# Performance work log

Hardware: AMD Instinct MI355X
Metric: run time of the kernel (lower is better)

## Reference

```python
import math
import jax, jax.numpy as jnp
import numpy as np

B, S, D = 2, 2048, 1024
H = 8
HD = D // H // 2            # 64, per-branch head dim
ROT = HD // 2               # 32, rotary rot_dim (RotaryEmbedding dim=head_dim//2)
DEPTH = 2
LAMBDA_INIT = 0.8 - 0.6 * math.exp(-0.3 * DEPTH)


def rope(t):
    # t: (b, s, heads, HD); rotate first ROT dims with interleaved pairs
    s = t.shape[1]
    inv = 1.0 / (10000.0 ** (jnp.arange(0, ROT, 2, dtype=jnp.float32) / ROT))  # (ROT/2,)
    freqs = jnp.arange(s, dtype=jnp.float32)[:, None] * inv                    # (s, ROT/2)
    freqs = jnp.repeat(freqs, 2, axis=-1)                                      # (s, ROT)
    cos = jnp.cos(freqs)[None, :, None, :]
    sin = jnp.sin(freqs)[None, :, None, :]
    tl, tr = t[..., :ROT], t[..., ROT:]
    xp = tl.reshape(tl.shape[:-1] + (ROT // 2, 2))
    rh = jnp.stack((-xp[..., 1], xp[..., 0]), axis=-1).reshape(tl.shape)
    return jnp.concatenate([tl * cos + rh * sin, tr], axis=-1)


def rmsnorm(x, w, b, eps=1e-8):
    return x * jax.lax.rsqrt(jnp.mean(x * x, axis=-1, keepdims=True) + eps) * w + b


def layernorm(x, w, b, eps=1e-5):
    m = jnp.mean(x, axis=-1, keepdims=True)
    v = jnp.mean((x - m) ** 2, axis=-1, keepdims=True)
    return (x - m) * jax.lax.rsqrt(v + eps) * w + b


def causal_attn(q, k, v):
    # q,k: (b,s,h,dqk)  v: (b,s,h,dv) -> (b,s,h,dv); flash default scale 1/sqrt(dqk)
    s = q.shape[1]
    scores = jnp.einsum('bqhd,bkhd->bhqk', q, k) / jnp.sqrt(jnp.asarray(q.shape[-1], q.dtype))
    mask = jnp.tril(jnp.ones((s, s), dtype=bool))
    scores = jnp.where(mask, scores, jnp.asarray(-jnp.inf, scores.dtype))
    p = jax.nn.softmax(scores, axis=-1)
    return jnp.einsum('bhqk,bkhe->bqhe', p, v)


def setup_inputs() -> dict:
    key = jax.random.key(0)
    ks = jax.random.split(key, 16)
    f32 = jnp.float32
    inp = {
        'x': jax.random.normal(ks[0], (B, S, D), dtype=f32),
        'sigmas': jax.random.normal(ks[1], (B, HD), dtype=f32),
        'w_qkv': jax.random.normal(ks[2], (D, 3 * D), dtype=f32) * 0.02,
        'w_out': jax.random.normal(ks[3], (D, D), dtype=f32) * 0.02,
        'lq1': jax.random.normal(ks[4], (HD,), dtype=f32) * 0.1,
        'lk1': jax.random.normal(ks[5], (HD,), dtype=f32) * 0.1,
        'lq2': jax.random.normal(ks[6], (HD,), dtype=f32) * 0.1,
        'lk2': jax.random.normal(ks[7], (HD,), dtype=f32) * 0.1,
        'ln_w': jnp.ones((2 * HD,), f32) + 0.02 * jax.random.normal(ks[8], (2 * HD,), dtype=f32),
        'ln_b': 0.02 * jax.random.normal(ks[9], (2 * HD,), dtype=f32),
        'lnq_w': jnp.ones((HD,), f32) + 0.02 * jax.random.normal(ks[10], (HD,), dtype=f32),
        'lnq_b': 0.02 * jax.random.normal(ks[11], (HD,), dtype=f32),
        'ln1_w': jnp.ones((D,), f32), 'ln1_b': jnp.zeros((D,), f32),
        'ln2_w': jnp.ones((D,), f32), 'ln2_b': jnp.zeros((D,), f32),
        'w1': jax.random.normal(ks[12], (D, 4 * D), dtype=f32) * 0.02,
        'b1': jnp.zeros((4 * D,), f32),
        'w2': jax.random.normal(ks[13], (4 * D, D), dtype=f32) * 0.02,
        'b2': jnp.zeros((D,), f32),
    }
    return inp


def reference(x, sigmas, w_qkv, w_out, lq1, lk1, lq2, lk2, ln_w, ln_b,
              lnq_w, lnq_b, ln1_w, ln1_b, ln2_w, ln2_b, w1, b1, w2, b2):
    b, s, d = x.shape
    qkv = x @ w_qkv
    q, k, v = jnp.split(qkv, 3, axis=-1)
    q = q.reshape(b, s, 2 * H, HD)
    k = k.reshape(b, s, 2 * H, HD)
    v = v.reshape(b, s, H, 2 * HD)
    q = rope(q)
    k = rope(k)
    q = q.reshape(b, s, H, 2, HD)
    k = k.reshape(b, s, H, 2, HD)
    q1, q2 = q[..., 0, :], q[..., 1, :]
    k1, k2 = k[..., 0, :], k[..., 1, :]
    sig = sigmas[:, None, None, :]  # (b,1,1,HD)
    attn1 = causal_attn(q1, k1, v)
    attn2 = causal_attn(rmsnorm(q2 + sig, lnq_w, lnq_b), rmsnorm(k2 + sig, lnq_w, lnq_b), v)
    lam = jnp.exp(jnp.sum(lq1 * lk1)) - jnp.exp(jnp.sum(lq2 * lk2)) + LAMBDA_INIT
    a = rmsnorm(attn1 - lam * attn2, ln_w, ln_b) * (1.0 - LAMBDA_INIT)
    a = a.reshape(b, s, d) @ w_out
    h = layernorm(a + x, ln1_w, ln1_b)
    ff = jax.nn.silu(h @ w1 + b1) @ w2 + b2
    return layernorm(ff + h, ln2_w, ln2_b)
```

## Files before the change

kernel.cpp:

```cpp
#include <hip/hip_runtime.h>
#include <math.h>
#include <stdint.h>

#define B_ 2
#define S_ 2048
#define D_ 1024
#define H_ 8
#define NT_ (B_*S_)

static constexpr float LAMBDA_INIT = 0.47071301834358415f;
static constexpr float ONE_MINUS_LI = 1.0f - 0.47071301834358415f;

typedef __attribute__((ext_vector_type(8))) short bf16x8;
typedef __attribute__((ext_vector_type(4))) float f32x4;

__device__ __forceinline__ unsigned short f2bf(float x) {
    union { float f; unsigned int u; } v; v.f = x;
    unsigned int r = v.u + 0x7fffu + ((v.u >> 16) & 1u);
    return (unsigned short)(r >> 16);
}
__device__ __forceinline__ float bf2f(unsigned short b) {
    union { unsigned int u; float f; } v; v.u = ((unsigned int)b) << 16;
    return v.f;
}

#define GLD16(gp, lp) __builtin_amdgcn_global_load_lds( \
    (const __attribute__((address_space(1))) void*)(gp), \
    (__attribute__((address_space(3))) void*)(lp), 16, 0, 0)

__global__ void lam_kernel(const float* __restrict__ lq1, const float* __restrict__ lk1,
                           const float* __restrict__ lq2, const float* __restrict__ lk2,
                           float* __restrict__ lam_out) {
    int t = threadIdx.x;
    float p1 = lq1[t] * lk1[t];
    float p2 = lq2[t] * lk2[t];
    for (int off = 32; off; off >>= 1) {
        p1 += __shfl_xor(p1, off);
        p2 += __shfl_xor(p2, off);
    }
    if (t == 0) lam_out[0] = expf(p1) - expf(p2) + LAMBDA_INIT;
}

__global__ __launch_bounds__(256) void convert_bf16(const float* __restrict__ in,
                                                    short* __restrict__ out) {
    const size_t i = ((size_t)blockIdx.x * 256 + threadIdx.x) * 4;
    float4 v = *(const float4*)(in + i);
    ushort4 o = make_ushort4(f2bf(v.x), f2bf(v.y), f2bf(v.z), f2bf(v.w));
    *(ushort4*)(out + i) = o;
}

__global__ __launch_bounds__(256) void transpose_to_bf16(const float* __restrict__ W,
                                                         short* __restrict__ WT,
                                                         int K, int N) {
    __shared__ float tile[32][33];
    const int t = threadIdx.x;
    const int k0 = blockIdx.y * 32, n0 = blockIdx.x * 32;
    const int r = t >> 3, c0 = (t & 7) * 4;
    float4 v = *(const float4*)(W + (size_t)(k0 + r) * N + n0 + c0);
    tile[r][c0 + 0] = v.x; tile[r][c0 + 1] = v.y;
    tile[r][c0 + 2] = v.z; tile[r][c0 + 3] = v.w;
    __syncthreads();
    ushort4 o = make_ushort4(f2bf(tile[c0 + 0][r]), f2bf(tile[c0 + 1][r]),
                             f2bf(tile[c0 + 2][r]), f2bf(tile[c0 + 3][r]));
    *(ushort4*)(WT + (size_t)(n0 + r) * K + k0 + c0) = o;
}

__global__ __launch_bounds__(256) void vtrans_kernel(const short* __restrict__ qkv_bf,
                                                     short* __restrict__ vt) {
    __shared__ short tile[32][34];
    const int s0 = blockIdx.x * 32, e0 = blockIdx.y * 32, bh = blockIdx.z;
    const int b = bh >> 3, h = bh & 7;
    const int t = threadIdx.x, r = t >> 3, c0 = (t & 7) * 4;
    ushort4 v = *(const ushort4*)(qkv_bf + (size_t)(b * S_ + s0 + r) * 3072 + 2048 + h * 128 + e0 + c0);
    tile[r][c0 + 0] = v.x; tile[r][c0 + 1] = v.y;
    tile[r][c0 + 2] = v.z; tile[r][c0 + 3] = v.w;
    __syncthreads();
    ushort4 o = make_ushort4((unsigned short)tile[c0 + 0][r], (unsigned short)tile[c0 + 1][r],
                             (unsigned short)tile[c0 + 2][r], (unsigned short)tile[c0 + 3][r]);
    *(ushort4*)(vt + ((size_t)bh * 128 + e0 + r) * S_ + s0 + c0) = o;
}

template <int EPI, int OUTBF>
__global__ __launch_bounds__(256) void gemm_bt(const short* __restrict__ A,
                                               const short* __restrict__ BT,
                                               const float* __restrict__ bias,
                                               void* __restrict__ Cout,
                                               int M, int N, int K) {
    __shared__ short As[128 * 32];
    __shared__ short Bs[128 * 32];
    const int t = threadIdx.x;
    const int w = t >> 6, l = t & 63;
    const int lr = l & 15, lg = l >> 4;
    const int row0 = blockIdx.y * 128, col0 = blockIdx.x * 128;
    const int wr = (w >> 1) * 64, wc = (w & 1) * 64;

    f32x4 acc[4][4];
#pragma unroll
    for (int i = 0; i < 4; ++i)
#pragma unroll
        for (int j = 0; j < 4; ++j) acc[i][j] = (f32x4){0.f, 0.f, 0.f, 0.f};

    const short* Ag = A + (size_t)(row0 + w * 32 + (l >> 2)) * K + (l & 3) * 8;
    const short* Bg = BT + (size_t)(col0 + w * 32 + (l >> 2)) * K + (l & 3) * 8;

    for (int k0 = 0; k0 < K; k0 += 32) {
        __syncthreads();
#pragma unroll
        for (int j = 0; j < 2; ++j) {
            GLD16(Ag + k0 + (size_t)j * 16 * K, As + (w * 2 + j) * 512);
            GLD16(Bg + k0 + (size_t)j * 16 * K, Bs + (w * 2 + j) * 512);
        }
        __syncthreads();

        bf16x8 af[4], bfr[4];
#pragma unroll
        for (int i = 0; i < 4; ++i)
            af[i] = *(const bf16x8*)(As + (wr + i * 16 + lr) * 32 + lg * 8);
#pragma unroll
        for (int j = 0; j < 4; ++j)
            bfr[j] = *(const bf16x8*)(Bs + (wc + j * 16 + lr) * 32 + lg * 8);
#pragma unroll
        for (int i = 0; i < 4; ++i)
#pragma unroll
            for (int j = 0; j < 4; ++j)
                acc[i][j] = __builtin_amdgcn_mfma_f32_16x16x32_bf16(af[i], bfr[j], acc[i][j], 0, 0, 0);
    }

#pragma unroll
    for (int i = 0; i < 4; ++i) {
#pragma unroll
        for (int j = 0; j < 4; ++j) {
            const int col = col0 + wc + j * 16 + lr;
            float bcol = (EPI >= 1) ? bias[col] : 0.f;
#pragma unroll
            for (int r = 0; r < 4; ++r) {
                const int row = row0 + wr + i * 16 + lg * 4 + r;
                float v = acc[i][j][r];
                if (EPI >= 1) v += bcol;
                if (EPI == 2) v = v / (1.0f + expf(-v));
                if (OUTBF) ((short*)Cout)[(size_t)row * N + col] = (short)f2bf(v);
                else       ((float*)Cout)[(size_t)row * N + col] = v;
            }
        }
    }
}

__global__ __launch_bounds__(256) void rope_kernel(const short* __restrict__ qkv,
                                                   const float* __restrict__ sigmas,
                                                   const float* __restrict__ lnq_w,
                                                   const float* __restrict__ lnq_b,
                                                   short* __restrict__ q1, short* __restrict__ q2n,
                                                   short* __restrict__ k1, short* __restrict__ k2n) {
    const int tok = blockIdx.x;
    const int b = tok >> 11, s = tok & 2047;
    const int t = threadIdx.x;
    const int hh = t >> 4;
    const int d0 = (t & 15) * 4;

    const short* qrow = qkv + (size_t)tok * 3072 + hh * 64 + d0;
    ushort4 qv = *(const ushort4*)qrow;
    ushort4 kv = *(const ushort4*)(qrow + 1024);
    float q[4] = {bf2f(qv.x), bf2f(qv.y), bf2f(qv.z), bf2f(qv.w)};
    float k[4] = {bf2f(kv.x), bf2f(kv.y), bf2f(kv.z), bf2f(kv.w)};

    if (d0 < 32) {
#pragma unroll
        for (int pr = 0; pr < 2; ++pr) {
            const int i = d0 / 2 + pr;
            float freq = (float)s * powf(10000.0f, -(float)i / 16.0f);
            float sn, c;
            sincosf(freq, &sn, &c);
            float x0 = q[2 * pr], x1 = q[2 * pr + 1];
            q[2 * pr]     = x0 * c - x1 * sn;
            q[2 * pr + 1] = x1 * c + x0 * sn;
            x0 = k[2 * pr]; x1 = k[2 * pr + 1];
            k[2 * pr]     = x0 * c - x1 * sn;
            k[2 * pr + 1] = x1 * c + x0 * sn;
        }
    }

    const int h = hh >> 1, j = hh & 1;
    const size_t obase = ((size_t)(b * H_ + h) * S_ + s) * 64 + d0;
    if (j == 0) {
        *(ushort4*)&q1[obase] = make_ushort4(f2bf(q[0]), f2bf(q[1]), f2bf(q[2]), f2bf(q[3]));
        *(ushort4*)&k1[obase] = make_ushort4(f2bf(k[0]), f2bf(k[1]), f2bf(k[2]), f2bf(k[3]));
    } else {
        float ssq_q = 0.f, ssq_k = 0.f;
#pragma unroll
        for (int i = 0; i < 4; ++i) {
            const float sg = sigmas[b * 64 + d0 + i];
            q[i] += sg; k[i] += sg;
            ssq_q += q[i] * q[i];
            ssq_k += k[i] * k[i];
        }
        for (int off = 1; off < 16; off <<= 1) {
            ssq_q += __shfl_xor(ssq_q, off, 16);
            ssq_k += __shfl_xor(ssq_k, off, 16);
        }
        const float rq = rsqrtf(ssq_q / 64.0f + 1e-8f);
        const float rk = rsqrtf(ssq_k / 64.0f + 1e-8f);
        float oq[4], ok[4];
#pragma unroll
        for (int i = 0; i < 4; ++i) {
            const float w = lnq_w[d0 + i], bb = lnq_b[d0 + i];
            oq[i] = q[i] * rq * w + bb;
            ok[i] = k[i] * rk * w + bb;
        }
        *(ushort4*)&q2n[obase] = make_ushort4(f2bf(oq[0]), f2bf(oq[1]), f2bf(oq[2]), f2bf(oq[3]));
        *(ushort4*)&k2n[obase] = make_ushort4(f2bf(ok[0]), f2bf(ok[1]), f2bf(ok[2]), f2bf(ok[3]));
    }
}

__device__ __forceinline__ void sm_update(f32x4 (&s)[4], float (&m)[4], float (&lsum)[4],
                                          f32x4 (&o)[8], short* __restrict__ Pw,
                                          const bool diag, const int qr0, const int k0,
                                          const int lr, const int lg) {
    float nm[4];
#pragma unroll
    for (int r = 0; r < 4; ++r) nm[r] = m[r];
#pragma unroll
    for (int ks = 0; ks < 4; ++ks) {
#pragma unroll
        for (int r = 0; r < 4; ++r) {
            float v = s[ks][r];
            if (diag && (k0 + ks * 16 + lr > qr0 + r)) v = -INFINITY;
            else v *= 0.125f;
            s[ks][r] = v;
            nm[r] = fmaxf(nm[r], v);
        }
    }
#pragma unroll
    for (int r = 0; r < 4; ++r) {
        nm[r] = fmaxf(nm[r], __shfl_xor(nm[r], 1));
        nm[r] = fmaxf(nm[r], __shfl_xor(nm[r], 2));
        nm[r] = fmaxf(nm[r], __shfl_xor(nm[r], 4));
        nm[r] = fmaxf(nm[r], __shfl_xor(nm[r], 8));
    }
    bool grow = false;
#pragma unroll
    for (int r = 0; r < 4; ++r) grow = grow || (nm[r] > m[r] + 8.0f);
    if (__any(grow)) {
        float al[4];
#pragma unroll
        for (int r = 0; r < 4; ++r) {
            al[r] = __expf(m[r] - nm[r]);
            m[r] = nm[r];
            lsum[r] *= al[r];
        }
#pragma unroll
        for (int es = 0; es < 8; ++es) {
#pragma unroll
            for (int r = 0; r < 4; ++r) o[es][r] *= al[r];
        }
    }
    float rs[4] = {0.f, 0.f, 0.f, 0.f};
#pragma unroll
    for (int ks = 0; ks < 4; ++ks) {
#pragma unroll
        for (int r = 0; r < 4; ++r) {
            float p = __expf(s[ks][r] - m[r]);
            rs[r] += p;
            Pw[(lg * 4 + r) * 72 + ks * 16 + lr] = (short)f2bf(p);
        }
    }
#pragma unroll
    for (int r = 0; r < 4; ++r) {
        rs[r] += __shfl_xor(rs[r], 1);
        rs[r] += __shfl_xor(rs[r], 2);
        rs[r] += __shfl_xor(rs[r], 4);
        rs[r] += __shfl_xor(rs[r], 8);
        lsum[r] += rs[r];
    }
}

__global__ __launch_bounds__(256, 3) void attn_part(const short* __restrict__ q1g,
                                                    const short* __restrict__ q2g,
                                                    const short* __restrict__ k1g,
                                                    const short* __restrict__ k2g,
                                                    const short* __restrict__ vt,
                                                    short* __restrict__ pO0,
                                                    short* __restrict__ pO1,
                                                    float* __restrict__ pml) {
    __shared__ short Ks1[64 * 72];
    __shared__ short Ks2[64 * 72];
    __shared__ short Vt[128 * 72];
    __shared__ short Ps[4][16 * 72];

    const int i = blockIdx.x;
    const int xcd = i & 7;
    const int slot = i >> 3;
    const int a = slot >> 6;
    const int j = slot & 63;
    const int qt = 31 - (j >> 1);
    const int part = j & 1;
    const int bh = xcd * 2 + a;
    const int q0 = qt * 64;
    const int t = threadIdx.x, w = t >> 6, l = t & 63;
    const int lr = l & 15, lg = l >> 4;

    const size_t kbase = (size_t)bh * S_ * 64;
    const size_t vbase = (size_t)bh * 128 * S_;

    bf16x8 qa1[2], qa2[2];
    {
        const size_t rb = kbase + (size_t)(q0 + w * 16 + lr) * 64;
#pragma unroll
        for (int dh = 0; dh < 2; ++dh) {
            qa1[dh] = *(const bf16x8*)(q1g + rb + dh * 32 + lg * 8);
            qa2[dh] = *(const bf16x8*)(q2g + rb + dh * 32 + lg * 8);
        }
    }

    const int nkt = qt + 1, mid = (nkt + 1) >> 1;
    const int kt0 = part ? mid : 0, kt1 = part ? nkt : mid;

    float m1[4], m2[4], l1[4], l2[4];
#pragma unroll
    for (int r = 0; r < 4; ++r) { m1[r] = -1e30f; m2[r] = -1e30f; l1[r] = 0.f; l2[r] = 0.f; }
    f32x4 o1[8], o2[8];
#pragma unroll
    for (int es = 0; es < 8; ++es) { o1[es] = (f32x4){0.f,0.f,0.f,0.f}; o2[es] = (f32x4){0.f,0.f,0.f,0.f}; }

    short* Pw = &Ps[w][0];
    const int qr0 = q0 + w * 16 + lg * 4;
    const int wrow_lo = q0 + w * 16;

    const int sr = t >> 2, sc = (t & 3) * 16;
    const int vr = t >> 1, vc = (t & 1) * 32;

    for (int kt = kt0; kt < kt1; ++kt) {
        const int k0 = kt * 64;
        __syncthreads();
        {
            const size_t g = kbase + (size_t)(k0 + sr) * 64 + sc;
            *(bf16x8*)(Ks1 + sr * 72 + sc)     = *(const bf16x8*)(k1g + g);
            *(bf16x8*)(Ks1 + sr * 72 + sc + 8) = *(const bf16x8*)(k1g + g + 8);
            *(bf16x8*)(Ks2 + sr * 72 + sc)     = *(const bf16x8*)(k2g + g);
            *(bf16x8*)(Ks2 + sr * 72 + sc + 8) = *(const bf16x8*)(k2g + g + 8);
            const size_t gv = vbase + (size_t)vr * S_ + k0 + vc;
#pragma unroll
            for (int jj = 0; jj < 4; ++jj)
                *(bf16x8*)(Vt + vr * 72 + vc + jj * 8) = *(const bf16x8*)(vt + gv + jj * 8);
        }
        __syncthreads();

        const bool diag = (k0 + 63 > wrow_lo);

        {
            f32x4 s[4];
#pragma unroll
            for (int ks = 0; ks < 4; ++ks) s[ks] = (f32x4){0.f,0.f,0.f,0.f};
#pragma unroll
            for (int ks = 0; ks < 4; ++ks)
#pragma unroll
                for (int dh = 0; dh < 2; ++dh) {
                    bf16x8 kf = *(const bf16x8*)(Ks1 + (ks * 16 + lr) * 72 + dh * 32 + lg * 8);
                    s[ks] = __builtin_amdgcn_mfma_f32_16x16x32_bf16(qa1[dh], kf, s[ks], 0, 0, 0);
                }
            sm_update(s, m1, l1, o1, Pw, diag, qr0, k0, lr, lg);
#pragma unroll
            for (int kb = 0; kb < 2; ++kb) {
                bf16x8 pf = *(const bf16x8*)(Pw + lr * 72 + kb * 32 + lg * 8);
#pragma unroll
                for (int es = 0; es < 8; ++es) {
                    bf16x8 vf = *(const bf16x8*)(Vt + (es * 16 + lr) * 72 + kb * 32 + lg * 8);
                    o1[es] = __builtin_amdgcn_mfma_f32_16x16x32_bf16(pf, vf, o1[es], 0, 0, 0);
                }
            }
        }
        {
            f32x4 s[4];
#pragma unroll
            for (int ks = 0; ks < 4; ++ks) s[ks] = (f32x4){0.f,0.f,0.f,0.f};
#pragma unroll
            for (int ks = 0; ks < 4; ++ks)
#pragma unroll
                for (int dh = 0; dh < 2; ++dh) {
                    bf16x8 kf = *(const bf16x8*)(Ks2 + (ks * 16 + lr) * 72 + dh * 32 + lg * 8);
                    s[ks] = __builtin_amdgcn_mfma_f32_16x16x32_bf16(qa2[dh], kf, s[ks], 0, 0, 0);
                }
            sm_update(s, m2, l2, o2, Pw, diag, qr0, k0, lr, lg);
#pragma unroll
            for (int kb = 0; kb < 2; ++kb) {
                bf16x8 pf = *(const bf16x8*)(Pw + lr * 72 + kb * 32 + lg * 8);
#pragma unroll
                for (int es = 0; es < 8; ++es) {
                    bf16x8 vf = *(const bf16x8*)(Vt + (es * 16 + lr) * 72 + kb * 32 + lg * 8);
                    o2[es] = __builtin_amdgcn_mfma_f32_16x16x32_bf16(pf, vf, o2[es], 0, 0, 0);
                }
            }
        }
    }

    {
        uint32_t* pO = (uint32_t*)(part ? pO1 : pO0);
        const size_t wb = (((size_t)bh * 32 + qt) * 4 + w) * 2048;
#pragma unroll
        for (int r = 0; r < 4; ++r) {
#pragma unroll
            for (int u = 0; u < 4; ++u) {
                uint32_t v1 = (uint32_t)f2bf(o1[2 * u][r]) | ((uint32_t)f2bf(o1[2 * u + 1][r]) << 16);
                pO[wb + (size_t)((r * 2 + 0) * 4 + u) * 64 + l] = v1;
                uint32_t v2 = (uint32_t)f2bf(o2[2 * u][r]) | ((uint32_t)f2bf(o2[2 * u + 1][r]) << 16);
                pO[wb + (size_t)((r * 2 + 1) * 4 + u) * 64 + l] = v2;
            }
        }
    }
    if (lr == 0) {
#pragma unroll
        for (int r = 0; r < 4; ++r) {
            const int q = q0 + w * 16 + lg * 4 + r;
            float4 v = make_float4(m1[r], l1[r], m2[r], l2[r]);
            *(float4*)&pml[(((size_t)part * 16 + bh) * S_ + q) * 4] = v;
        }
    }
}

__global__ __launch_bounds__(256) void attn_combine(const short* __restrict__ pO0,
                                                    const short* __restrict__ pO1,
                                                    const float* __restrict__ pml,
                                                    const float* __restrict__ lamp,
                                                    const float* __restrict__ ln_w,
                                                    const float* __restrict__ ln_b,
                                                    short* __restrict__ arms) {
    const int tok = blockIdx.x;
    const int b = tok >> 11, q = tok & 2047;
    const int t = threadIdx.x;
    const int h = t >> 5, ln32 = t & 31, e0 = ln32 * 4;
    const int bh = b * H_ + h;
    const float lam = lamp[0];

    float4 mla = *(const float4*)&pml[(((size_t)0 * 16 + bh) * S_ + q) * 4];
    float4 mlb = *(const float4*)&pml[(((size_t)1 * 16 + bh) * S_ + q) * 4];

    const float m1 = fmaxf(mla.x, mlb.x);
    const float aa1 = __expf(mla.x - m1), ab1 = __expf(mlb.x - m1);
    const float il1 = 1.0f / (aa1 * mla.y + ab1 * mlb.y);
    const float m2 = fmaxf(mla.z, mlb.z);
    const float aa2 = __expf(mla.z - m2), ab2 = __expf(mlb.z - m2);
    const float il2 = 1.0f / (aa2 * mla.w + ab2 * mlb.w);

    const int qt = q >> 6, w = (q >> 4) & 3, lg = (q >> 2) & 3, r = q & 3;
    const int es = ln32 >> 2, u = es >> 1, half = es & 1;
    const int lane0 = lg * 16 + (ln32 & 3) * 4;
    const size_t wb = (((size_t)bh * 32 + qt) * 4 + w) * 2048;
    const uint32_t* P0 = (const uint32_t*)pO0;
    const uint32_t* P1 = (const uint32_t*)pO1;
    const uint4 a1  = *(const uint4*)&P0[wb + (size_t)((r * 2 + 0) * 4 + u) * 64 + lane0];
    const uint4 b1v = *(const uint4*)&P1[wb + (size_t)((r * 2 + 0) * 4 + u) * 64 + lane0];
    const uint4 a2  = *(const uint4*)&P0[wb + (size_t)((r * 2 + 1) * 4 + u) * 64 + lane0];
    const uint4 b2v = *(const uint4*)&P1[wb + (size_t)((r * 2 + 1) * 4 + u) * 64 + lane0];
    const int sh = 16 * half;

    float comb[4]; float ssq = 0.f;
    {
        const uint32_t aw1[4] = {a1.x, a1.y, a1.z, a1.w};
        const uint32_t bw1[4] = {b1v.x, b1v.y, b1v.z, b1v.w};
        const uint32_t aw2[4] = {a2.x, a2.y, a2.z, a2.w};
        const uint32_t bw2[4] = {b2v.x, b2v.y, b2v.z, b2v.w};
#pragma unroll
        for (int i = 0; i < 4; ++i) {
            const float O1 = (aa1 * bf2f((unsigned short)(aw1[i] >> sh)) +
                              ab1 * bf2f((unsigned short)(bw1[i] >> sh))) * il1;
            const float O2 = (aa2 * bf2f((unsigned short)(aw2[i] >> sh)) +
                              ab2 * bf2f((unsigned short)(bw2[i] >> sh))) * il2;
            const float c = O1 - lam * O2;
            comb[i] = c; ssq += c * c;
        }
    }
    for (int off = 1; off < 32; off <<= 1) ssq += __shfl_xor(ssq, off, 32);
    const float rms = rsqrtf(ssq / 128.0f + 1e-8f);

    ushort4 o;
    unsigned short* op = (unsigned short*)&o;
#pragma unroll
    for (int i = 0; i < 4; ++i) {
        const int e = e0 + i;
        op[i] = f2bf((comb[i] * rms * ln_w[e] + ln_b[e]) * ONE_MINUS_LI);
    }
    *(ushort4*)&arms[(size_t)tok * 1024 + h * 128 + e0] = o;
}

template <int WB>
__global__ __launch_bounds__(256) void add_ln_kernel(const float* __restrict__ X,
                                                     const float* __restrict__ Y,
                                                     const float* __restrict__ w,
                                                     const float* __restrict__ bvec,
                                                     float* __restrict__ out,
                                                     short* __restrict__ out_bf,
                                                     float eps) {
    const int row = blockIdx.x;
    const int t = threadIdx.x;
    __shared__ float red[4];

    float4 xv = *(const float4*)&X[(size_t)row * 1024 + t * 4];
    float4 yv = *(const float4*)&Y[(size_t)row * 1024 + t * 4];
    float v[4] = {xv.x + yv.x, xv.y + yv.y, xv.z + yv.z, xv.w + yv.w};

    float s = v[0] + v[1] + v[2] + v[3];
    for (int off = 1; off < 64; off <<= 1) s += __shfl_xor(s, off);
    if ((t & 63) == 0) red[t >> 6] = s;
    __syncthreads();
    const float mean = (red[0] + red[1] + red[2] + red[3]) * (1.0f / 1024.0f);

    float sq = 0.f;
#pragma unroll
    for (int i = 0; i < 4; ++i) { const float d = v[i] - mean; sq += d * d; }
    __syncthreads();
    for (int off = 1; off < 64; off <<= 1) sq += __shfl_xor(sq, off);
    if ((t & 63) == 0) red[t >> 6] = sq;
    __syncthreads();
    const float var = (red[0] + red[1] + red[2] + red[3]) * (1.0f / 1024.0f);
    const float rstd = rsqrtf(var + eps);

    float o[4];
#pragma unroll
    for (int i = 0; i < 4; ++i)
        o[i] = (v[i] - mean) * rstd * w[t * 4 + i] + bvec[t * 4 + i];
    *(float4*)&out[(size_t)row * 1024 + t * 4] = make_float4(o[0], o[1], o[2], o[3]);
    if (WB) {
        *(ushort4*)&out_bf[(size_t)row * 1024 + t * 4] =
            make_ushort4(f2bf(o[0]), f2bf(o[1]), f2bf(o[2]), f2bf(o[3]));
    }
}

extern "C" void kernel_launch(void* const* d_in, const int* in_sizes, int n_in,
                              void* d_out, int out_size, void* d_ws, size_t ws_size,
                              hipStream_t stream) {
    const float* x      = (const float*)d_in[0];
    const float* sigmas = (const float*)d_in[1];
    const float* w_qkv  = (const float*)d_in[2];
    const float* w_out  = (const float*)d_in[3];
    const float* lq1    = (const float*)d_in[4];
    const float* lk1    = (const float*)d_in[5];
    const float* lq2    = (const float*)d_in[6];
    const float* lk2    = (const float*)d_in[7];
    const float* ln_w   = (const float*)d_in[8];
    const float* ln_b   = (const float*)d_in[9];
    const float* lnq_w  = (const float*)d_in[10];
    const float* lnq_b  = (const float*)d_in[11];
    const float* ln1_w  = (const float*)d_in[12];
    const float* ln1_b  = (const float*)d_in[13];
    const float* ln2_w  = (const float*)d_in[14];
    const float* ln2_b  = (const float*)d_in[15];
    const float* w1     = (const float*)d_in[16];
    const float* b1     = (const float*)d_in[17];
    const float* w2     = (const float*)d_in[18];
    const float* b2     = (const float*)d_in[19];

    char* ws = (char*)d_ws;
    short* x_bf    = (short*)(ws + 0);
    short* vt      = (short*)(ws + 0);
    short* w_qkvT  = (short*)(ws + 8388608);
    short* w_outT  = (short*)(ws + 14680064);
    short* w1T     = (short*)(ws + 16777216);
    short* w2T     = (short*)(ws + 25165824);
    short* qkv_bf  = (short*)(ws + 33554432);
    short* pO0     = (short*)(ws + 33554432);
    float* pml     = (float*)(ws + 50331648);
    short* q1      = (short*)(ws + 58720256);
    short* q2n     = (short*)(ws + 62914560);
    short* k1      = (short*)(ws + 67108864);
    short* k2n     = (short*)(ws + 71303168);
    short* arms    = (short*)(ws + 75497472);
    short* pO1     = (short*)(ws + 83886080);
    float* a_f32   = (float*)(ws + 83886080);
    float* h_f32   = (float*)(ws + 33554432);
    short* h_bf    = (short*)(ws + 50331648);
    short* ffh     = (short*)(ws + 58720256);
    float* ff      = (float*)(ws + 0);
    float* lam     = (float*)(ws + 100663296);

    lam_kernel<<<1, 64, 0, stream>>>(lq1, lk1, lq2, lk2, lam);

    convert_bf16<<<4096, 256, 0, stream>>>(x, x_bf);
    transpose_to_bf16<<<dim3(3072 / 32, 1024 / 32), 256, 0, stream>>>(w_qkv, w_qkvT, 1024, 3072);
    transpose_to_bf16<<<dim3(1024 / 32, 1024 / 32), 256, 0, stream>>>(w_out, w_outT, 1024, 1024);
    transpose_to_bf16<<<dim3(4096 / 32, 1024 / 32), 256, 0, stream>>>(w1, w1T, 1024, 4096);
    transpose_to_bf16<<<dim3(1024 / 32, 4096 / 32), 256, 0, stream>>>(w2, w2T, 4096, 1024);

    gemm_bt<0, 1><<<dim3(3072 / 128, 4096 / 128), 256, 0, stream>>>(x_bf, w_qkvT, nullptr,
                                                                    qkv_bf, NT_, 3072, 1024);

    rope_kernel<<<NT_, 256, 0, stream>>>(qkv_bf, sigmas, lnq_w, lnq_b, q1, q2n, k1, k2n);
    vtrans_kernel<<<dim3(S_ / 32, 4, 16), 256, 0, stream>>>(qkv_bf, vt);

    attn_part<<<1024, 256, 0, stream>>>(q1, q2n, k1, k2n, vt, pO0, pO1, pml);
    attn_combine<<<NT_, 256, 0, stream>>>(pO0, pO1, pml, lam, ln_w, ln_b, arms);

    gemm_bt<0, 0><<<dim3(1024 / 128, 4096 / 128), 256, 0, stream>>>(arms, w_outT, nullptr,
                                                                    a_f32, NT_, 1024, 1024);

    add_ln_kernel<1><<<NT_, 256, 0, stream>>>(a_f32, x, ln1_w, ln1_b, h_f32, h_bf, 1e-5f);

    gemm_bt<2, 1><<<dim3(4096 / 128, 4096 / 128), 256, 0, stream>>>(h_bf, w1T, b1,
                                                                    ffh, NT_, 4096, 1024);

    gemm_bt<1, 0><<<dim3(1024 / 128, 4096 / 128), 256, 0, stream>>>(ffh, w2T, b2,
                                                                    ff, NT_, 1024, 4096);

    add_ln_kernel<0><<<NT_, 256, 0, stream>>>(ff, h_f32, ln2_w, ln2_b, (float*)d_out,
                                              nullptr, 1e-5f);
}
```

Measured before the change: 382.4 us.

## Fuse prep kernels, add split-K and XCD block remap to GEMMs, prioritize MFMA

Merges the x-to-bf16 conversion and four weight transposes into a single launch. The GEMM gains an XCD-aware block remap and a split-K mode for the two N=1024 GEMMs, which launch 512 blocks instead of 256 to fill more CUs. The two partial sums are added inside new residual-layernorm kernels, which also fold in the b2 bias and read h back as bf16. Attention raises wave priority around its MFMA sections. The residual h is now kept only as bf16, which adds rounding error, and the extra partial buffers add memory traffic.

```diff
diff --git a/kernel.cpp b/kernel.cpp
--- a/kernel.cpp
+++ b/kernel.cpp
@@ -41,20 +41,33 @@
     if (t == 0) lam_out[0] = expf(p1) - expf(p2) + LAMBDA_INIT;
 }
 
-__global__ __launch_bounds__(256) void convert_bf16(const float* __restrict__ in,
-                                                    short* __restrict__ out) {
-    const size_t i = ((size_t)blockIdx.x * 256 + threadIdx.x) * 4;
-    float4 v = *(const float4*)(in + i);
-    ushort4 o = make_ushort4(f2bf(v.x), f2bf(v.y), f2bf(v.z), f2bf(v.w));
-    *(ushort4*)(out + i) = o;
-}
-
-__global__ __launch_bounds__(256) void transpose_to_bf16(const float* __restrict__ W,
-                                                         short* __restrict__ WT,
-                                                         int K, int N) {
+__global__ __launch_bounds__(256) void prep_kernel(const float* __restrict__ x,
+                                                   const float* __restrict__ w_qkv,
+                                                   const float* __restrict__ w_out,
+                                                   const float* __restrict__ w1,
+                                                   const float* __restrict__ w2,
+                                                   short* __restrict__ x_bf,
+                                                   short* __restrict__ w_qkvT,
+                                                   short* __restrict__ w_outT,
+                                                   short* __restrict__ w1T,
+                                                   short* __restrict__ w2T) {
+    const int z = blockIdx.x;
+    if (z >= 12288) {
+        const size_t i = ((size_t)(z - 12288) * 256 + threadIdx.x) * 4;
+        float4 v = *(const float4*)(x + i);
+        *(ushort4*)(x_bf + i) = make_ushort4(f2bf(v.x), f2bf(v.y), f2bf(v.z), f2bf(v.w));
+        return;
+    }
+    const float* W; short* WT; int K, N, zz;
+    if (z < 3072)      { W = w_qkv; WT = w_qkvT; K = 1024; N = 3072; zz = z; }
+    else if (z < 4096) { W = w_out; WT = w_outT; K = 1024; N = 1024; zz = z - 3072; }
+    else if (z < 8192) { W = w1;    WT = w1T;    K = 1024; N = 4096; zz = z - 4096; }
+    else               { W = w2;    WT = w2T;    K = 4096; N = 1024; zz = z - 8192; }
+    const int nx = N >> 5;
+    const int bx = zz % nx, by = zz / nx;
     __shared__ float tile[32][33];
     const int t = threadIdx.x;
-    const int k0 = blockIdx.y * 32, n0 = blockIdx.x * 32;
+    const int k0 = by * 32, n0 = bx * 32;
     const int r = t >> 3, c0 = (t & 7) * 4;
     float4 v = *(const float4*)(W + (size_t)(k0 + r) * N + n0 + c0);
     tile[r][c0 + 0] = v.x; tile[r][c0 + 1] = v.y;
@@ -80,18 +93,27 @@
     *(ushort4*)(vt + ((size_t)bh * 128 + e0 + r) * S_ + s0 + c0) = o;
 }
 
-template <int EPI, int OUTBF>
+template <int EPI, int OUTBF, int SPLITK>
 __global__ __launch_bounds__(256) void gemm_bt(const short* __restrict__ A,
                                                const short* __restrict__ BT,
                                                const float* __restrict__ bias,
-                                               void* __restrict__ Cout,
-                                               int M, int N, int K) {
+                                               void* __restrict__ C0,
+                                               void* __restrict__ C1,
+                                               int M, int N, int Kfull, int Ksub) {
     __shared__ short As[128 * 32];
     __shared__ short Bs[128 * 32];
     const int t = threadIdx.x;
     const int w = t >> 6, l = t & 63;
     const int lr = l & 15, lg = l >> 4;
-    const int row0 = blockIdx.y * 128, col0 = blockIdx.x * 128;
+
+    const int GX = gridDim.x;
+    const int nwg = GX * gridDim.y;
+    int flat = blockIdx.y * GX + blockIdx.x;
+    flat = (flat & 7) * (nwg >> 3) + (flat >> 3);
+    int part = 0;
+    if (SPLITK) { const int per = nwg >> 1; part = flat / per; flat = flat % per; }
+    const int bx = flat % GX, by = flat / GX;
+    const int row0 = by * 128, col0 = bx * 128;
     const int wr = (w >> 1) * 64, wc = (w & 1) * 64;
 
     f32x4 acc[4][4];
@@ -100,15 +122,15 @@
 #pragma unroll
         for (int j = 0; j < 4; ++j) acc[i][j] = (f32x4){0.f, 0.f, 0.f, 0.f};
 
-    const short* Ag = A + (size_t)(row0 + w * 32 + (l >> 2)) * K + (l & 3) * 8;
-    const short* Bg = BT + (size_t)(col0 + w * 32 + (l >> 2)) * K + (l & 3) * 8;
-
-    for (int k0 = 0; k0 < K; k0 += 32) {
+    const short* Ag = A + (size_t)part * Ksub + (size_t)(row0 + w * 32 + (l >> 2)) * Kfull + (l & 3) * 8;
+    const short* Bg = BT + (size_t)part * Ksub + (size_t)(col0 + w * 32 + (l >> 2)) * Kfull + (l & 3) * 8;
+
+    for (int k0 = 0; k0 < Ksub; k0 += 32) {
         __syncthreads();
 #pragma unroll
         for (int j = 0; j < 2; ++j) {
-            GLD16(Ag + k0 + (size_t)j * 16 * K, As + (w * 2 + j) * 512);
-            GLD16(Bg + k0 + (size_t)j * 16 * K, Bs + (w * 2 + j) * 512);
+            GLD16(Ag + k0 + (size_t)j * 16 * Kfull, As + (w * 2 + j) * 512);
+            GLD16(Bg + k0 + (size_t)j * 16 * Kfull, Bs + (w * 2 + j) * 512);
         }
         __syncthreads();
 
@@ -126,6 +148,7 @@
                 acc[i][j] = __builtin_amdgcn_mfma_f32_16x16x32_bf16(af[i], bfr[j], acc[i][j], 0, 0, 0);
     }
 
+    void* Cout = (SPLITK && part) ? C1 : C0;
 #pragma unroll
     for (int i = 0; i < 4; ++i) {
 #pragma unroll
@@ -350,6 +373,7 @@
             f32x4 s[4];
 #pragma unroll
             for (int ks = 0; ks < 4; ++ks) s[ks] = (f32x4){0.f,0.f,0.f,0.f};
+            __builtin_amdgcn_s_setprio(1);
 #pragma unroll
             for (int ks = 0; ks < 4; ++ks)
 #pragma unroll
@@ -357,7 +381,9 @@
                     bf16x8 kf = *(const bf16x8*)(Ks1 + (ks * 16 + lr) * 72 + dh * 32 + lg * 8);
                     s[ks] = __builtin_amdgcn_mfma_f32_16x16x32_bf16(qa1[dh], kf, s[ks], 0, 0, 0);
                 }
+            __builtin_amdgcn_s_setprio(0);
             sm_update(s, m1, l1, o1, Pw, diag, qr0, k0, lr, lg);
+            __builtin_amdgcn_s_setprio(1);
 #pragma unroll
             for (int kb = 0; kb < 2; ++kb) {
                 bf16x8 pf = *(const bf16x8*)(Pw + lr * 72 + kb * 32 + lg * 8);
@@ -367,11 +393,13 @@
                     o1[es] = __builtin_amdgcn_mfma_f32_16x16x32_bf16(pf, vf, o1[es], 0, 0, 0);
                 }
             }
+            __builtin_amdgcn_s_setprio(0);
         }
         {
             f32x4 s[4];
 #pragma unroll
             for (int ks = 0; ks < 4; ++ks) s[ks] = (f32x4){0.f,0.f,0.f,0.f};
+            __builtin_amdgcn_s_setprio(1);
 #pragma unroll
             for (int ks = 0; ks < 4; ++ks)
 #pragma unroll
@@ -379,7 +407,9 @@
                     bf16x8 kf = *(const bf16x8*)(Ks2 + (ks * 16 + lr) * 72 + dh * 32 + lg * 8);
                     s[ks] = __builtin_amdgcn_mfma_f32_16x16x32_bf16(qa2[dh], kf, s[ks], 0, 0, 0);
                 }
+            __builtin_amdgcn_s_setprio(0);
             sm_update(s, m2, l2, o2, Pw, diag, qr0, k0, lr, lg);
+            __builtin_amdgcn_s_setprio(1);
 #pragma unroll
             for (int kb = 0; kb < 2; ++kb) {
                 bf16x8 pf = *(const bf16x8*)(Pw + lr * 72 + kb * 32 + lg * 8);
@@ -389,6 +419,7 @@
                     o2[es] = __builtin_amdgcn_mfma_f32_16x16x32_bf16(pf, vf, o2[es], 0, 0, 0);
                 }
             }
+            __builtin_amdgcn_s_setprio(0);
         }
     }
 
@@ -481,21 +512,21 @@
     *(ushort4*)&arms[(size_t)tok * 1024 + h * 128 + e0] = o;
 }
 
-template <int WB>
-__global__ __launch_bounds__(256) void add_ln_kernel(const float* __restrict__ X,
-                                                     const float* __restrict__ Y,
-                                                     const float* __restrict__ w,
-                                                     const float* __restrict__ bvec,
-                                                     float* __restrict__ out,
-                                                     short* __restrict__ out_bf,
-                                                     float eps) {
+__global__ __launch_bounds__(256) void add_ln1_kernel(const float* __restrict__ A0,
+                                                      const float* __restrict__ A1,
+                                                      const float* __restrict__ X,
+                                                      const float* __restrict__ w,
+                                                      const float* __restrict__ bvec,
+                                                      short* __restrict__ out_bf) {
     const int row = blockIdx.x;
     const int t = threadIdx.x;
     __shared__ float red[4];
 
+    float4 a0 = *(const float4*)&A0[(size_t)row * 1024 + t * 4];
+    float4 a1 = *(const float4*)&A1[(size_t)row * 1024 + t * 4];
     float4 xv = *(const float4*)&X[(size_t)row * 1024 + t * 4];
-    float4 yv = *(const float4*)&Y[(size_t)row * 1024 + t * 4];
-    float v[4] = {xv.x + yv.x, xv.y + yv.y, xv.z + yv.z, xv.w + yv.w};
+    float v[4] = {a0.x + a1.x + xv.x, a0.y + a1.y + xv.y,
+                  a0.z + a1.z + xv.z, a0.w + a1.w + xv.w};
 
     float s = v[0] + v[1] + v[2] + v[3];
     for (int off = 1; off < 64; off <<= 1) s += __shfl_xor(s, off);
@@ -511,17 +542,55 @@
     if ((t & 63) == 0) red[t >> 6] = sq;
     __syncthreads();
     const float var = (red[0] + red[1] + red[2] + red[3]) * (1.0f / 1024.0f);
-    const float rstd = rsqrtf(var + eps);
+    const float rstd = rsqrtf(var + 1e-5f);
+
+    ushort4 o;
+    unsigned short* op = (unsigned short*)&o;
+#pragma unroll
+    for (int i = 0; i < 4; ++i)
+        op[i] = f2bf((v[i] - mean) * rstd * w[t * 4 + i] + bvec[t * 4 + i]);
+    *(ushort4*)&out_bf[(size_t)row * 1024 + t * 4] = o;
+}
+
+__global__ __launch_bounds__(256) void add_ln2_kernel(const float* __restrict__ F0,
+                                                      const float* __restrict__ F1,
+                                                      const float* __restrict__ bias,
+                                                      const short* __restrict__ Hbf,
+                                                      const float* __restrict__ w,
+                                                      const float* __restrict__ bvec,
+                                                      float* __restrict__ out) {
+    const int row = blockIdx.x;
+    const int t = threadIdx.x;
+    __shared__ float red[4];
+
+    float4 f0 = *(const float4*)&F0[(size_t)row * 1024 + t * 4];
+    float4 f1 = *(const float4*)&F1[(size_t)row * 1024 + t * 4];
+    float4 bv = *(const float4*)&bias[t * 4];
+    ushort4 hv = *(const ushort4*)&Hbf[(size_t)row * 1024 + t * 4];
+    float v[4] = {f0.x + f1.x + bv.x + bf2f(hv.x), f0.y + f1.y + bv.y + bf2f(hv.y),
+                  f0.z + f1.z + bv.z + bf2f(hv.z), f0.w + f1.w + bv.w + bf2f(hv.w)};
+
+    float s = v[0] + v[1] + v[2] + v[3];
+    for (int off = 1; off < 64; off <<= 1) s += __shfl_xor(s, off);
+    if ((t & 63) == 0) red[t >> 6] = s;
+    __syncthreads();
+    const float mean = (red[0] + red[1] + red[2] + red[3]) * (1.0f / 1024.0f);
+
+    float sq = 0.f;
+#pragma unroll
+    for (int i = 0; i < 4; ++i) { const float d = v[i] - mean; sq += d * d; }
+    __syncthreads();
+    for (int off = 1; off < 64; off <<= 1) sq += __shfl_xor(sq, off);
+    if ((t & 63) == 0) red[t >> 6] = sq;
+    __syncthreads();
+    const float var = (red[0] + red[1] + red[2] + red[3]) * (1.0f / 1024.0f);
+    const float rstd = rsqrtf(var + 1e-5f);
 
     float o[4];
 #pragma unroll
     for (int i = 0; i < 4; ++i)
         o[i] = (v[i] - mean) * rstd * w[t * 4 + i] + bvec[t * 4 + i];
     *(float4*)&out[(size_t)row * 1024 + t * 4] = make_float4(o[0], o[1], o[2], o[3]);
-    if (WB) {
-        *(ushort4*)&out_bf[(size_t)row * 1024 + t * 4] =
-            make_ushort4(f2bf(o[0]), f2bf(o[1]), f2bf(o[2]), f2bf(o[3]));
-    }
 }
 
 extern "C" void kernel_launch(void* const* d_in, const int* in_sizes, int n_in,
@@ -551,6 +620,7 @@
     char* ws = (char*)d_ws;
     short* x_bf    = (short*)(ws + 0);
     short* vt      = (short*)(ws + 0);
+    short* h_bf    = (short*)(ws + 0);
     short* w_qkvT  = (short*)(ws + 8388608);
     short* w_outT  = (short*)(ws + 14680064);
     short* w1T     = (short*)(ws + 16777216);
@@ -558,29 +628,25 @@
     short* qkv_bf  = (short*)(ws + 33554432);
     short* pO0     = (short*)(ws + 33554432);
     float* pml     = (float*)(ws + 50331648);
+    float* a_p0    = (float*)(ws + 33554432);
     short* q1      = (short*)(ws + 58720256);
     short* q2n     = (short*)(ws + 62914560);
     short* k1      = (short*)(ws + 67108864);
     short* k2n     = (short*)(ws + 71303168);
-    short* arms    = (short*)(ws + 75497472);
-    short* pO1     = (short*)(ws + 83886080);
-    float* a_f32   = (float*)(ws + 83886080);
-    float* h_f32   = (float*)(ws + 33554432);
-    short* h_bf    = (short*)(ws + 50331648);
-    short* ffh     = (short*)(ws + 58720256);
-    float* ff      = (float*)(ws + 0);
+    float* a_p1    = (float*)(ws + 58720256);
+    short* pO1     = (short*)(ws + 75497472);
+    short* arms    = (short*)(ws + 92274688);
+    short* ffh     = (short*)(ws + 33554432);
+    float* ff_p0   = (float*)(ws + 67108864);
+    float* ff_p1   = (float*)(ws + 83886080);
     float* lam     = (float*)(ws + 100663296);
 
     lam_kernel<<<1, 64, 0, stream>>>(lq1, lk1, lq2, lk2, lam);
-
-    convert_bf16<<<4096, 256, 0, stream>>>(x, x_bf);
-    transpose_to_bf16<<<dim3(3072 / 32, 1024 / 32), 256, 0, stream>>>(w_qkv, w_qkvT, 1024, 3072);
-    transpose_to_bf16<<<dim3(1024 / 32, 1024 / 32), 256, 0, stream>>>(w_out, w_outT, 1024, 1024);
-    transpose_to_bf16<<<dim3(4096 / 32, 1024 / 32), 256, 0, stream>>>(w1, w1T, 1024, 4096);
-    transpose_to_bf16<<<dim3(1024 / 32, 4096 / 32), 256, 0, stream>>>(w2, w2T, 4096, 1024);
-
-    gemm_bt<0, 1><<<dim3(3072 / 128, 4096 / 128), 256, 0, stream>>>(x_bf, w_qkvT, nullptr,
-                                                                    qkv_bf, NT_, 3072, 1024);
+    prep_kernel<<<16384, 256, 0, stream>>>(x, w_qkv, w_out, w1, w2,
+                                           x_bf, w_qkvT, w_outT, w1T, w2T);
+
+    gemm_bt<0, 1, 0><<<dim3(24, 32), 256, 0, stream>>>(x_bf, w_qkvT, nullptr,
+                                                       qkv_bf, nullptr, NT_, 3072, 1024, 1024);
 
     rope_kernel<<<NT_, 256, 0, stream>>>(qkv_bf, sigmas, lnq_w, lnq_b, q1, q2n, k1, k2n);
     vtrans_kernel<<<dim3(S_ / 32, 4, 16), 256, 0, stream>>>(qkv_bf, vt);
@@ -588,17 +654,17 @@
     attn_part<<<1024, 256, 0, stream>>>(q1, q2n, k1, k2n, vt, pO0, pO1, pml);
     attn_combine<<<NT_, 256, 0, stream>>>(pO0, pO1, pml, lam, ln_w, ln_b, arms);
 
-    gemm_bt<0, 0><<<dim3(1024 / 128, 4096 / 128), 256, 0, stream>>>(arms, w_outT, nullptr,
-                                                                    a_f32, NT_, 1024, 1024);
-
-    add_ln_kernel<1><<<NT_, 256, 0, stream>>>(a_f32, x, ln1_w, ln1_b, h_f32, h_bf, 1e-5f);
-
-    gemm_bt<2, 1><<<dim3(4096 / 128, 4096 / 128), 256, 0, stream>>>(h_bf, w1T, b1,
-                                                                    ffh, NT_, 4096, 1024);
-
-    gemm_bt<1, 0><<<dim3(1024 / 128, 4096 / 128), 256, 0, stream>>>(ffh, w2T, b2,
-                                                                    ff, NT_, 1024, 4096);
-
-    add_ln_kernel<0><<<NT_, 256, 0, stream>>>(ff, h_f32, ln2_w, ln2_b, (float*)d_out,
-                                              nullptr, 1e-5f);
-}
+    gemm_bt<0, 0, 1><<<dim3(8, 64), 256, 0, stream>>>(arms, w_outT, nullptr,
+                                                      a_p0, a_p1, NT_, 1024, 1024, 512);
+
+    add_ln1_kernel<<<NT_, 256, 0, stream>>>(a_p0, a_p1, x, ln1_w, ln1_b, h_bf);
+
+    gemm_bt<2, 1, 0><<<dim3(32, 32), 256, 0, stream>>>(h_bf, w1T, b1,
+                                                       ffh, nullptr, NT_, 4096, 1024, 1024);
+
+    gemm_bt<0, 0, 1><<<dim3(8, 64), 256, 0, stream>>>(ffh, w2T, nullptr,
+                                                      ff_p0, ff_p1, NT_, 1024, 4096, 2048);
+
+    add_ln2_kernel<<<NT_, 256, 0, stream>>>(ff_p0, ff_p1, b2, h_bf, ln2_w, ln2_b,
+                                            (float*)d_out);
+}
```

New measurement: 336.9 us. 1.14x faster.
